# Kernel optimization log

Hardware: AMD Instinct MI355X
Metric: run time of the kernel (lower is better)

The kernel has to match this reference:

```python
import jax, jax.numpy as jnp
import numpy as np

N_NODES = 50000
N_EDGES = 1600000
IN_DIM = 128
HIDDEN = 256
N_CLASSES = 2
N_GRAPHS = 512
BN_EPS = 1e-5


def setup_inputs() -> dict:
    key = jax.random.key(0)
    ks = jax.random.split(key, 12)
    x = jax.random.normal(ks[0], (N_NODES, IN_DIM), dtype=jnp.float32)
    edge_index = jax.random.randint(ks[1], (2, N_EDGES), 0, N_NODES, dtype=jnp.int64)
    batch = jnp.sort(jax.random.randint(ks[2], (N_NODES,), 0, N_GRAPHS, dtype=jnp.int64))
    s1 = 1.0 / np.sqrt(IN_DIM)
    s2 = 1.0 / np.sqrt(HIDDEN)
    return {
        "x": x,
        "edge_index": edge_index,
        "batch": batch,
        # GIN MLP: Linear(in,hidden) -> BN -> ReLU -> Linear(hidden,hidden)
        "W1": jax.random.uniform(ks[3], (IN_DIM, HIDDEN), jnp.float32, -s1, s1),
        "b1": jnp.zeros((HIDDEN,), jnp.float32),
        "g1": jnp.ones((HIDDEN,), jnp.float32),
        "be1": jnp.zeros((HIDDEN,), jnp.float32),
        "W2": jax.random.uniform(ks[4], (HIDDEN, HIDDEN), jnp.float32, -s2, s2),
        "b2": jnp.zeros((HIDDEN,), jnp.float32),
        # attention gate: Linear(hidden, 1)
        "Wg": jax.random.uniform(ks[5], (HIDDEN, 1), jnp.float32, -s2, s2),
        "bg": jnp.zeros((1,), jnp.float32),
        # head: BN(hidden) -> Dropout(eval: identity) -> Linear(hidden, n_classes)
        "g2": jnp.ones((HIDDEN,), jnp.float32),
        "be2": jnp.zeros((HIDDEN,), jnp.float32),
        "Wh": jax.random.uniform(ks[6], (HIDDEN, N_CLASSES), jnp.float32, -s2, s2),
        "bh": jnp.zeros((N_CLASSES,), jnp.float32),
    }


def _batchnorm(h, gamma, beta):
    # training-mode BN: batch statistics over axis 0 (biased variance, as torch)
    mu = jnp.mean(h, axis=0)
    var = jnp.mean(jnp.square(h - mu), axis=0)
    return gamma * (h - mu) * jax.lax.rsqrt(var + BN_EPS) + beta


def reference(x, edge_index, batch, W1, b1, g1, be1, W2, b2, Wg, bg, g2, be2, Wh, bh):
    src, dst = edge_index[0], edge_index[1]
    # GINConv (eps=0): agg_i = sum_{j->i} x_j ; h = MLP(x + agg)
    agg = jax.ops.segment_sum(x[src], dst, num_segments=N_NODES)  # [N, in_dim]
    h = x + agg
    h = h @ W1 + b1                      # [N, hidden]
    h = jax.nn.relu(_batchnorm(h, g1, be1))
    h = h @ W2 + b2                      # [N, hidden]
    h = jax.nn.relu(h)                   # outer F.relu in forward
    # AttentionalAggregation: segment softmax of gate, weighted sum per graph
    gate = h @ Wg + bg                   # [N, 1]
    m = jax.ops.segment_max(gate, batch, num_segments=N_GRAPHS)  # [G, 1]
    e = jnp.exp(gate - m[batch])
    s = jax.ops.segment_sum(e, batch, num_segments=N_GRAPHS)     # [G, 1]
    alpha = e / s[batch]                 # [N, 1]
    pooled = jax.ops.segment_sum(alpha * h, batch, num_segments=N_GRAPHS)  # [G, hidden]
    # head: BN -> (Dropout eval = identity) -> Linear -> log_softmax
    z = _batchnorm(pooled, g2, be2) @ Wh + bh  # [G, n_classes]
    return jax.nn.log_softmax(z, axis=-1)
```

## Files before the change

### kernel.cpp

```cpp
#include <hip/hip_runtime.h>

typedef unsigned int u32;
typedef unsigned short ushort_t;
typedef __attribute__((ext_vector_type(8))) short bf16x8;
typedef __attribute__((ext_vector_type(4))) float f32x4;

#define PCAP 3072
#define OVFCAP 1600000

__device__ __forceinline__ float bf2f_lo(u32 u){
  union{u32 i; float f;} v; v.i = u<<16; return v.f;
}
__device__ __forceinline__ float bf2f_hi(u32 u){
  union{u32 i; float f;} v; v.i = u & 0xFFFF0000u; return v.f;
}
__device__ __forceinline__ float bf2f_s(ushort_t u){
  union{u32 i; float f;} v; v.i = ((u32)u)<<16; return v.f;
}
__device__ __forceinline__ u32 pack2bf(float a, float b){
  union{float f; u32 i;} va, vb; va.f=a; vb.f=b;
  u32 ra = (va.i + 0x7FFF + ((va.i>>16)&1)) >> 16;
  u32 rb = (vb.i + 0x7FFF + ((vb.i>>16)&1)) & 0xFFFF0000u;
  return ra | rb;
}
__device__ __forceinline__ ushort_t f2bf1(float f){
  union{float f; u32 i;} v; v.f=f;
  u32 r = v.i + 0x7FFF + ((v.i>>16)&1);
  return (ushort_t)(r>>16);
}

__global__ __launch_bounds__(256) void prep(const float* __restrict__ x, u32* __restrict__ xb, long nconv,
                                            const float* __restrict__ W1, ushort_t* __restrict__ W1t,
                                            const float* __restrict__ W2, ushort_t* __restrict__ W2t,
                                            int* __restrict__ bcursor, int* __restrict__ ovf_cnt, int NB){
  long blk = blockIdx.x;
  int tid = threadIdx.x;
  if(blk < nconv){
    long i = blk*256 + tid;
    float4 v = ((const float4*)x)[i];
    uint2 o; o.x = pack2bf(v.x, v.y); o.y = pack2bf(v.z, v.w);
    ((uint2*)xb)[i] = o;
  } else if(blk < nconv + 256){
    int n = (int)(blk - nconv);
    for(int k = tid; k < 128; k += 256) W1t[(size_t)n*128 + k] = f2bf1(W1[(size_t)k*256 + n]);
  } else if(blk < nconv + 512){
    int n = (int)(blk - nconv - 256);
    for(int k = tid; k < 256; k += 256) W2t[(size_t)n*256 + k] = f2bf1(W2[(size_t)k*256 + n]);
  } else {
    for(int i = tid; i < NB*16; i += 256) bcursor[i] = 0;
    if(tid == 0) *ovf_cnt = 0;
  }
}

__global__ __launch_bounds__(256) void binscatter_direct(const int* __restrict__ src, const int* __restrict__ dst,
                                                         int* __restrict__ bcursor, u32* __restrict__ pairs,
                                                         int* __restrict__ ovf, int* __restrict__ ovf_cnt,
                                                         int E, int N, int NB){
  __shared__ int hist[1024];
  __shared__ int base[1024];
  int e0 = blockIdx.x*8192;
  int e1 = min(e0+8192, E);
  for(int i=threadIdx.x; i<NB; i+=256) hist[i]=0;
  __syncthreads();
  for(int i=e0+threadIdx.x; i<e1; i+=256){
    int d = dst[i];
    if((u32)d >= (u32)N) d = 0;
    atomicAdd(&hist[d>>6], 1);
  }
  __syncthreads();
  for(int i=threadIdx.x; i<NB; i+=256){
    int c = hist[i];
    base[i] = c ? atomicAdd(&bcursor[i*16], c) : 0;
    hist[i] = 0;
  }
  __syncthreads();
  for(int i=e0+threadIdx.x; i<e1; i+=256){
    int d = dst[i]; if((u32)d >= (u32)N) d = 0;
    int s = src[i]; if((u32)s >= (u32)N) s = 0;
    int b = d>>6;
    int loc = atomicAdd(&hist[b], 1);
    int pos = base[b] + loc;
    if(pos < PCAP){
      pairs[(size_t)b*PCAP + pos] = (u32)s | (((u32)(d & 63))<<17);
    } else {
      int o = atomicAdd(ovf_cnt, 1);
      if(o < OVFCAP){ ovf[2*o] = s; ovf[2*o+1] = d; }
    }
  }
}

__global__ __launch_bounds__(512) void gather_bucket(const u32* __restrict__ xb,
                                                     const u32* __restrict__ pairs,
                                                     const int* __restrict__ bcursor,
                                                     const int* __restrict__ ovf, const int* __restrict__ ovf_cnt,
                                                     u32* __restrict__ h0b, int N){
  __shared__ int lsrc[PCAP];
  __shared__ int dcnt[64];
  __shared__ int dstart[65];
  __shared__ int dcur[64];
  __shared__ int s_ovfn;
  int b = blockIdx.x;
  int tid = threadIdx.x;
  int cnt = bcursor[b*16];
  if(cnt < 0) cnt = 0;
  int cl = min(cnt, PCAP);
  if(tid < 64) dcnt[tid] = 0;
  if(tid == 0){ int o = *ovf_cnt; s_ovfn = (o < 0) ? 0 : min(o, OVFCAP); }
  __syncthreads();
  const u32* mypairs = pairs + (size_t)b*PCAP;
  for(int i=tid; i<cl; i+=512){
    u32 u = mypairs[i];
    atomicAdd(&dcnt[(u>>17)&63], 1);
  }
  __syncthreads();
  if(tid==0){
    int run=0;
    #pragma unroll
    for(int j=0;j<64;j++){ dstart[j]=run; dcur[j]=run; run+=dcnt[j]; }
    dstart[64]=run;
  }
  __syncthreads();
  for(int i=tid; i<cl; i+=512){
    u32 u = mypairs[i];
    int pos = atomicAdd(&dcur[(u>>17)&63], 1);
    lsrc[pos] = (int)(u & 0x1FFFFu);
  }
  __syncthreads();
  int ovfn = s_ovfn;
  const uint4* xr = (const uint4*)xb;
  int slot = tid >> 4;
  int c = tid & 15;
  for(int pass=0; pass<2; pass++){
    int r = pass*32 + slot;
    int node = b*64 + r;
    if(node >= N) continue;
    uint4 xv = xr[(size_t)node*16 + c];
    float acc[8] = {
      bf2f_lo(xv.x), bf2f_hi(xv.x), bf2f_lo(xv.y), bf2f_hi(xv.y),
      bf2f_lo(xv.z), bf2f_hi(xv.z), bf2f_lo(xv.w), bf2f_hi(xv.w) };
    int ds = dstart[r], de = dstart[r+1];
    int j = ds;
    for(; j+8 <= de; j += 8){
      int s0=lsrc[j+0], s1=lsrc[j+1], s2=lsrc[j+2], s3=lsrc[j+3];
      int s4=lsrc[j+4], s5=lsrc[j+5], s6=lsrc[j+6], s7=lsrc[j+7];
      uint4 v0 = xr[(size_t)s0*16 + c];
      uint4 v1 = xr[(size_t)s1*16 + c];
      uint4 v2 = xr[(size_t)s2*16 + c];
      uint4 v3 = xr[(size_t)s3*16 + c];
      uint4 v4 = xr[(size_t)s4*16 + c];
      uint4 v5 = xr[(size_t)s5*16 + c];
      uint4 v6 = xr[(size_t)s6*16 + c];
      uint4 v7 = xr[(size_t)s7*16 + c];
      acc[0]+=bf2f_lo(v0.x)+bf2f_lo(v1.x)+bf2f_lo(v2.x)+bf2f_lo(v3.x)
             +bf2f_lo(v4.x)+bf2f_lo(v5.x)+bf2f_lo(v6.x)+bf2f_lo(v7.x);
      acc[1]+=bf2f_hi(v0.x)+bf2f_hi(v1.x)+bf2f_hi(v2.x)+bf2f_hi(v3.x)
             +bf2f_hi(v4.x)+bf2f_hi(v5.x)+bf2f_hi(v6.x)+bf2f_hi(v7.x);
      acc[2]+=bf2f_lo(v0.y)+bf2f_lo(v1.y)+bf2f_lo(v2.y)+bf2f_lo(v3.y)
             +bf2f_lo(v4.y)+bf2f_lo(v5.y)+bf2f_lo(v6.y)+bf2f_lo(v7.y);
      acc[3]+=bf2f_hi(v0.y)+bf2f_hi(v1.y)+bf2f_hi(v2.y)+bf2f_hi(v3.y)
             +bf2f_hi(v4.y)+bf2f_hi(v5.y)+bf2f_hi(v6.y)+bf2f_hi(v7.y);
      acc[4]+=bf2f_lo(v0.z)+bf2f_lo(v1.z)+bf2f_lo(v2.z)+bf2f_lo(v3.z)
             +bf2f_lo(v4.z)+bf2f_lo(v5.z)+bf2f_lo(v6.z)+bf2f_lo(v7.z);
      acc[5]+=bf2f_hi(v0.z)+bf2f_hi(v1.z)+bf2f_hi(v2.z)+bf2f_hi(v3.z)
             +bf2f_hi(v4.z)+bf2f_hi(v5.z)+bf2f_hi(v6.z)+bf2f_hi(v7.z);
      acc[6]+=bf2f_lo(v0.w)+bf2f_lo(v1.w)+bf2f_lo(v2.w)+bf2f_lo(v3.w)
             +bf2f_lo(v4.w)+bf2f_lo(v5.w)+bf2f_lo(v6.w)+bf2f_lo(v7.w);
      acc[7]+=bf2f_hi(v0.w)+bf2f_hi(v1.w)+bf2f_hi(v2.w)+bf2f_hi(v3.w)
             +bf2f_hi(v4.w)+bf2f_hi(v5.w)+bf2f_hi(v6.w)+bf2f_hi(v7.w);
    }
    for(; j < de; j++){
      int s = lsrc[j];
      uint4 v = xr[(size_t)s*16 + c];
      acc[0]+=bf2f_lo(v.x); acc[1]+=bf2f_hi(v.x);
      acc[2]+=bf2f_lo(v.y); acc[3]+=bf2f_hi(v.y);
      acc[4]+=bf2f_lo(v.z); acc[5]+=bf2f_hi(v.z);
      acc[6]+=bf2f_lo(v.w); acc[7]+=bf2f_hi(v.w);
    }
    if(ovfn > 0){
      for(int i=0;i<ovfn;i++){
        int s = ovf[2*i], d = ovf[2*i+1];
        if(d == node){
          if((u32)s >= (u32)N) s = 0;
          uint4 v = xr[(size_t)s*16 + c];
          acc[0]+=bf2f_lo(v.x); acc[1]+=bf2f_hi(v.x);
          acc[2]+=bf2f_lo(v.y); acc[3]+=bf2f_hi(v.y);
          acc[4]+=bf2f_lo(v.z); acc[5]+=bf2f_hi(v.z);
          acc[6]+=bf2f_lo(v.w); acc[7]+=bf2f_hi(v.w);
        }
      }
    }
    uint4 o;
    o.x = pack2bf(acc[0],acc[1]); o.y = pack2bf(acc[2],acc[3]);
    o.z = pack2bf(acc[4],acc[5]); o.w = pack2bf(acc[6],acc[7]);
    ((uint4*)h0b)[(size_t)node*16 + c] = o;
  }
}

template<int K, bool BNA, bool RELUOUT, bool GATE, bool ABF16, bool OUTBF16, bool STATS>
__global__ __launch_bounds__(512) void gemm_mfma(const void* __restrict__ Ap, const ushort_t* __restrict__ Wt,
                                                 const float* __restrict__ bias,
                                                 const float* __restrict__ scale, const float* __restrict__ shift,
                                                 void* __restrict__ Cp, int M,
                                                 const float* __restrict__ Wg, const float* __restrict__ bg,
                                                 float* __restrict__ gate,
                                                 float* __restrict__ psum, float* __restrict__ pq, int NS){
  __shared__ uint4 Al[8*129];
  __shared__ uint4 Bl[8*257];
  __shared__ float gacc[128];
  __shared__ float sstat[512];
  const int tid  = threadIdx.x;
  const int lane = tid & 63;
  const int wave = tid >> 6;
  const int lm   = lane & 15;
  const int q    = lane >> 4;
  const int mhalf= wave >> 2;
  const int nq   = wave & 3;
  const int m0   = blockIdx.x * 128;

  if(GATE && tid < 128) gacc[tid] = 0.f;
  if(STATS){ sstat[tid] = 0.f; }

  f32x4 acc[4][4];
  #pragma unroll
  for(int i=0;i<4;i++)
    #pragma unroll
    for(int j=0;j<4;j++) acc[i][j] = (f32x4){0.f,0.f,0.f,0.f};

  for(int k0=0; k0<K; k0+=64){
    #pragma unroll
    for(int i=0;i<2;i++){
      int idx = tid*2 + i;
      int m = idx >> 3, c = idx & 7;
      int grow = m0 + m;
      int kk = k0 + c*8;
      uint4 v = make_uint4(0,0,0,0);
      if(ABF16){
        if(grow < M) v = *(const uint4*)((const ushort_t*)Ap + (size_t)grow*K + kk);
        if(BNA){
          float f0=bf2f_lo(v.x), f1=bf2f_hi(v.x), f2=bf2f_lo(v.y), f3=bf2f_hi(v.y);
          float f4=bf2f_lo(v.z), f5=bf2f_hi(v.z), f6=bf2f_lo(v.w), f7=bf2f_hi(v.w);
          float4 s0 = *(const float4*)(scale+kk),  s1 = *(const float4*)(scale+kk+4);
          float4 t0 = *(const float4*)(shift+kk),  t1 = *(const float4*)(shift+kk+4);
          f0=fmaxf(fmaf(s0.x,f0,t0.x),0.f); f1=fmaxf(fmaf(s0.y,f1,t0.y),0.f);
          f2=fmaxf(fmaf(s0.z,f2,t0.z),0.f); f3=fmaxf(fmaf(s0.w,f3,t0.w),0.f);
          f4=fmaxf(fmaf(s1.x,f4,t1.x),0.f); f5=fmaxf(fmaf(s1.y,f5,t1.y),0.f);
          f6=fmaxf(fmaf(s1.z,f6,t1.z),0.f); f7=fmaxf(fmaf(s1.w,f7,t1.w),0.f);
          v.x = pack2bf(f0,f1); v.y = pack2bf(f2,f3);
          v.z = pack2bf(f4,f5); v.w = pack2bf(f6,f7);
        }
      } else {
        float4 u0 = make_float4(0,0,0,0), u1 = make_float4(0,0,0,0);
        if(grow < M){
          u0 = *(const float4*)((const float*)Ap + (size_t)grow*K + kk);
          u1 = *(const float4*)((const float*)Ap + (size_t)grow*K + kk + 4);
        }
        if(BNA){
          float4 s0 = *(const float4*)(scale+kk),  s1 = *(const float4*)(scale+kk+4);
          float4 t0 = *(const float4*)(shift+kk),  t1 = *(const float4*)(shift+kk+4);
          u0.x=fmaxf(fmaf(s0.x,u0.x,t0.x),0.f); u0.y=fmaxf(fmaf(s0.y,u0.y,t0.y),0.f);
          u0.z=fmaxf(fmaf(s0.z,u0.z,t0.z),0.f); u0.w=fmaxf(fmaf(s0.w,u0.w,t0.w),0.f);
          u1.x=fmaxf(fmaf(s1.x,u1.x,t1.x),0.f); u1.y=fmaxf(fmaf(s1.y,u1.y,t1.y),0.f);
          u1.z=fmaxf(fmaf(s1.z,u1.z,t1.z),0.f); u1.w=fmaxf(fmaf(s1.w,u1.w,t1.w),0.f);
        }
        v.x = pack2bf(u0.x,u0.y); v.y = pack2bf(u0.z,u0.w);
        v.z = pack2bf(u1.x,u1.y); v.w = pack2bf(u1.z,u1.w);
      }
      Al[c*129 + m] = v;
    }
    #pragma unroll
    for(int i=0;i<4;i++){
      int idx = tid*4 + i;
      int n = idx >> 3, c = idx & 7;
      Bl[c*257 + n] = *(const uint4*)(Wt + (size_t)n*K + k0 + c*8);
    }
    __syncthreads();
    #pragma unroll
    for(int ks=0; ks<2; ks++){
      int cc = ks*4 + q;
      bf16x8 af[4], bfr[4];
      #pragma unroll
      for(int mi=0; mi<4; mi++)
        af[mi] = *((const bf16x8*)&Al[cc*129 + mhalf*64 + mi*16 + lm]);
      #pragma unroll
      for(int ni=0; ni<4; ni++)
        bfr[ni] = *((const bf16x8*)&Bl[cc*257 + nq*64 + ni*16 + lm]);
      #pragma unroll
      for(int mi=0; mi<4; mi++)
        #pragma unroll
        for(int ni=0; ni<4; ni++)
          acc[mi][ni] = __builtin_amdgcn_mfma_f32_16x16x32_bf16(af[mi], bfr[ni], acc[mi][ni], 0, 0, 0);
    }
    __syncthreads();
  }

  float bb[4], wgv[4];
  float cs[4] = {0.f,0.f,0.f,0.f};
  float cq[4] = {0.f,0.f,0.f,0.f};
  #pragma unroll
  for(int ni=0; ni<4; ni++){
    int col = nq*64 + ni*16 + lm;
    bb[ni] = bias[col];
    if(GATE) wgv[ni] = Wg[col];
  }
  #pragma unroll
  for(int mi=0; mi<4; mi++){
    int rowloc0 = mhalf*64 + mi*16 + q*4;
    float gp[4] = {0.f,0.f,0.f,0.f};
    #pragma unroll
    for(int ni=0; ni<4; ni++){
      int col = nq*64 + ni*16 + lm;
      f32x4 o = acc[mi][ni];
      #pragma unroll
      for(int r=0; r<4; r++){
        float v = o[r] + bb[ni];
        if(RELUOUT) v = fmaxf(v, 0.f);
        int row = m0 + rowloc0 + r;
        if(row < M){
          if(OUTBF16) ((ushort_t*)Cp)[(size_t)row*256 + col] = f2bf1(v);
          else        ((float*)Cp)[(size_t)row*256 + col] = v;
          if(STATS){ cs[ni] += v; cq[ni] = fmaf(v, v, cq[ni]); }
        }
        if(GATE) gp[r] = fmaf(v, wgv[ni], gp[r]);
      }
    }
    if(GATE){
      #pragma unroll
      for(int r=0; r<4; r++){
        if(m0 + rowloc0 + r < M) atomicAdd(&gacc[rowloc0 + r], gp[r]);
      }
    }
  }
  if(STATS){
    __syncthreads();
    #pragma unroll
    for(int ni=0; ni<4; ni++){
      int col = nq*64 + ni*16 + lm;
      atomicAdd(&sstat[col], cs[ni]);
      atomicAdd(&sstat[256+col], cq[ni]);
    }
    __syncthreads();
    if(tid < 256){
      psum[(size_t)tid*NS + blockIdx.x] = sstat[tid];
      pq[(size_t)tid*NS + blockIdx.x]   = sstat[256+tid];
    }
  }
  if(GATE){
    __syncthreads();
    if(tid < 128){
      int row = m0 + tid;
      if(row < M) gate[row] = gacc[tid] + bg[0];
    }
  }
}

__global__ __launch_bounds__(256) void col_stats2(const float* __restrict__ h, float* __restrict__ psum,
                                                  float* __restrict__ pq, int M, int rpb, int nblk){
  int b = blockIdx.x;
  int g = threadIdx.x >> 6;
  int lane = threadIdx.x & 63;
  int c0 = lane*4;
  int r0 = b*rpb;
  int r1 = min(r0+rpb, M);
  float4 s4 = make_float4(0.f,0.f,0.f,0.f);
  float4 q4 = make_float4(0.f,0.f,0.f,0.f);
  for(int r=r0+g; r<r1; r+=4){
    float4 v = *(const float4*)(h + (size_t)r*256 + c0);
    s4.x+=v.x; s4.y+=v.y; s4.z+=v.z; s4.w+=v.w;
    q4.x=fmaf(v.x,v.x,q4.x); q4.y=fmaf(v.y,v.y,q4.y);
    q4.z=fmaf(v.z,v.z,q4.z); q4.w=fmaf(v.w,v.w,q4.w);
  }
  __shared__ float ls[1024];
  __shared__ float lq[1024];
  *(float4*)&ls[g*256+c0] = s4;
  *(float4*)&lq[g*256+c0] = q4;
  __syncthreads();
  if(threadIdx.x < 64){
    #pragma unroll
    for(int j=0;j<4;j++){
      int c = c0+j;
      float s = ls[c]+ls[256+c]+ls[512+c]+ls[768+c];
      float q = lq[c]+lq[256+c]+lq[512+c]+lq[768+c];
      psum[(size_t)c*nblk + b] = s;
      pq[(size_t)c*nblk + b]   = q;
    }
  }
}

__global__ __launch_bounds__(512) void stats_fin(const float* __restrict__ psum, const float* __restrict__ pq,
                                                 const float* __restrict__ gamma, const float* __restrict__ beta,
                                                 float* __restrict__ scale, float* __restrict__ shift,
                                                 int nblk, int NS, float invM){
  __shared__ float red[512];
  int t = threadIdx.x;
  const float* src = (t<256) ? (psum + (size_t)t*NS) : (pq + (size_t)(t-256)*NS);
  float s = 0.f;
  int i = 0;
  for(; i+4 <= nblk; i += 4){
    float4 v = *(const float4*)(src+i);
    s += v.x+v.y+v.z+v.w;
  }
  for(; i < nblk; i++) s += src[i];
  red[t]=s; __syncthreads();
  if(t<256){
    float mu  = red[t]*invM;
    float var = fmaxf(red[256+t]*invM - mu*mu, 0.f);
    float sc  = gamma[t] * rsqrtf(var + 1e-5f);
    scale[t]=sc; shift[t]=fmaf(-mu, sc, beta[t]);
  }
}

__global__ __launch_bounds__(512) void pool_k(const ushort_t* __restrict__ h2b, const float* __restrict__ gate,
                                              const int* __restrict__ batch, float* __restrict__ pooled, int N){
  int g = blockIdx.x;
  __shared__ int sb[2];
  __shared__ float red[8];
  __shared__ float s_m, s_inv;
  __shared__ float la[256];
  __shared__ float sa0[512];
  __shared__ float sa1[512];
  int t = threadIdx.x;
  if(t < 2){
    int target = g + t;
    int lo=0, hi=N;
    while(lo<hi){ int mid=(lo+hi)>>1; if(batch[mid] < target) lo=mid+1; else hi=mid; }
    sb[t] = lo;
  }
  __syncthreads();
  int beg = sb[0], end = sb[1];
  float mx = -1e30f;
  for(int i=beg+t; i<end; i+=512) mx = fmaxf(mx, gate[i]);
  #pragma unroll
  for(int d=32; d>0; d>>=1) mx = fmaxf(mx, __shfl_down(mx, d, 64));
  if((t&63)==0) red[t>>6] = mx;
  __syncthreads();
  if(t==0){
    float m = red[0];
    #pragma unroll
    for(int w=1; w<8; w++) m = fmaxf(m, red[w]);
    s_m = m;
  }
  __syncthreads();
  float m = s_m;
  float s = 0.f;
  for(int i=beg+t; i<end; i+=512) s += expf(gate[i]-m);
  #pragma unroll
  for(int d=32; d>0; d>>=1) s += __shfl_down(s, d, 64);
  if((t&63)==0) red[t>>6] = s;
  __syncthreads();
  if(t==0){
    float tot = 0.f;
    #pragma unroll
    for(int w=0; w<8; w++) tot += red[w];
    s_inv = (tot > 0.f) ? 1.f/tot : 0.f;
  }
  __syncthreads();
  float inv = s_inv;
  const u32* h2w = (const u32*)h2b;
  int colpair = t & 127;
  int rowgrp  = t >> 7;
  float a0 = 0.f, a1 = 0.f;
  for(int ci=beg; ci<end; ci+=256){
    int chunk = min(256, end-ci);
    if(t < 256) la[t] = (t < chunk) ? expf(gate[ci+t]-m)*inv : 0.f;
    __syncthreads();
    for(int j=rowgrp; j<chunk; j+=4){
      u32 h = h2w[(size_t)(ci+j)*128 + colpair];
      float w = la[j];
      a0 = fmaf(w, bf2f_lo(h), a0);
      a1 = fmaf(w, bf2f_hi(h), a1);
    }
    __syncthreads();
  }
  sa0[t] = a0; sa1[t] = a1;
  __syncthreads();
  if(t < 128){
    float r0 = sa0[t] + sa0[128+t] + sa0[256+t] + sa0[384+t];
    float r1 = sa1[t] + sa1[128+t] + sa1[256+t] + sa1[384+t];
    pooled[g*256 + t*2]   = r0;
    pooled[g*256 + t*2+1] = r1;
  }
}

__global__ __launch_bounds__(256) void head_k(const float* __restrict__ pooled,
                                              const float* __restrict__ sc2, const float* __restrict__ sh2,
                                              const float* __restrict__ Wh, const float* __restrict__ bh,
                                              float* __restrict__ out, int G){
  int w = (blockIdx.x*256 + threadIdx.x) >> 6;
  int l = threadIdx.x & 63;
  if(w >= G) return;
  float4 v  = *(const float4*)(pooled + (size_t)w*256 + l*4);
  float4 sc = *(const float4*)(sc2 + l*4);
  float4 sh = *(const float4*)(sh2 + l*4);
  float vv[4] = { fmaf(sc.x,v.x,sh.x), fmaf(sc.y,v.y,sh.y), fmaf(sc.z,v.z,sh.z), fmaf(sc.w,v.w,sh.w) };
  float4 w0 = *(const float4*)(Wh + (size_t)l*8);
  float4 w1 = *(const float4*)(Wh + (size_t)l*8 + 4);
  float a0 = vv[0]*w0.x + vv[1]*w0.z + vv[2]*w1.x + vv[3]*w1.z;
  float a1 = vv[0]*w0.y + vv[1]*w0.w + vv[2]*w1.y + vv[3]*w1.w;
  #pragma unroll
  for(int d=32; d>0; d>>=1){ a0 += __shfl_down(a0,d,64); a1 += __shfl_down(a1,d,64); }
  if(l==0){
    float z0 = a0 + bh[0];
    float z1 = a1 + bh[1];
    float mz = fmaxf(z0,z1);
    float lse = mz + logf(expf(z0-mz) + expf(z1-mz));
    out[w*2]   = z0 - lse;
    out[w*2+1] = z1 - lse;
  }
}

extern "C" void kernel_launch(void* const* d_in, const int* in_sizes, int n_in,
                              void* d_out, int out_size, void* d_ws, size_t ws_size,
                              hipStream_t stream){
  const float* x   = (const float*)d_in[0];
  const int*   ei  = (const int*)d_in[1];
  const int*   bat = (const int*)d_in[2];
  const float* W1  = (const float*)d_in[3];
  const float* b1  = (const float*)d_in[4];
  const float* g1  = (const float*)d_in[5];
  const float* be1 = (const float*)d_in[6];
  const float* W2  = (const float*)d_in[7];
  const float* b2  = (const float*)d_in[8];
  const float* Wg  = (const float*)d_in[9];
  const float* bg  = (const float*)d_in[10];
  const float* g2  = (const float*)d_in[11];
  const float* be2 = (const float*)d_in[12];
  const float* Wh  = (const float*)d_in[13];
  const float* bh  = (const float*)d_in[14];

  const int N = in_sizes[0] / 128;
  const int E = in_sizes[1] / 2;
  const int G = out_size / 2;
  const int NB = (N + 63) >> 6;
  const int gblocks = (N + 127)/128;
  const int NS1 = (gblocks + 7) & ~7;
  const int NBLK2 = 64;

  char* ws = (char*)d_ws;
  u32*   h0b    = (u32*)ws;
  u32*   xb     = (u32*)(ws + 12800000);
  u32*   pairs  = (u32*)(ws + 25600000);
  int*   bcursor= (int*)(ws + 35210240);
  int*   ovf_cnt= (int*)(ws + 35275776);
  int*   ovf    = (int*)(ws + 35276032);
  ushort_t* h2b = (ushort_t*)ws;
  u32*   h1b    = (u32*)(ws + 51200000);
  char*  p2 = ws + 102400000;
  float* psum1 = (float*)p2;          p2 += 256*NS1*4;
  float* pq1   = (float*)p2;          p2 += 256*NS1*4;
  float* psum2 = (float*)p2;          p2 += 256*NBLK2*4;
  float* pq2   = (float*)p2;          p2 += 256*NBLK2*4;
  float* sc1   = (float*)p2;          p2 += 1024;
  float* sh1   = (float*)p2;          p2 += 1024;
  float* sc2   = (float*)p2;          p2 += 1024;
  float* sh2   = (float*)p2;          p2 += 1024;
  float* gate  = (float*)p2;          p2 += (size_t)N*4 + 4096;
  float* pooled= (float*)p2;          p2 += (size_t)G*256*4;
  ushort_t* W1t = (ushort_t*)p2;      p2 += 256*128*2;
  ushort_t* W2t = (ushort_t*)p2;      p2 += 256*256*2;

  const int* src = ei;
  const int* dst = ei + E;

  long nconv = (long)N*128/4/256;
  prep<<<(int)(nconv + 512 + 1), 256, 0, stream>>>(x, xb, nconv, W1, W1t, W2, W2t, bcursor, ovf_cnt, NB);

  int nchunk = (E + 8191)/8192;
  binscatter_direct<<<nchunk, 256, 0, stream>>>(src, dst, bcursor, pairs, ovf, ovf_cnt, E, N, NB);
  gather_bucket<<<NB, 512, 0, stream>>>(xb, pairs, bcursor, ovf, ovf_cnt, h0b, N);

  gemm_mfma<128,false,false,false,true,true,true><<<gblocks, 512, 0, stream>>>(
      h0b, W1t, b1, nullptr, nullptr, h1b, N, nullptr, nullptr, nullptr, psum1, pq1, NS1);
  stats_fin<<<1, 512, 0, stream>>>(psum1, pq1, g1, be1, sc1, sh1, gblocks, NS1, 1.0f/(float)N);
  gemm_mfma<256,true,true,true,true,true,false><<<gblocks, 512, 0, stream>>>(
      h1b, W2t, b2, sc1, sh1, h2b, N, Wg, bg, gate, nullptr, nullptr, 0);

  pool_k<<<G, 512, 0, stream>>>(h2b, gate, bat, pooled, N);
  int rpb2 = (G + NBLK2 - 1)/NBLK2;
  col_stats2<<<NBLK2, 256, 0, stream>>>(pooled, psum2, pq2, G, rpb2, NBLK2);
  stats_fin<<<1, 512, 0, stream>>>(psum2, pq2, g2, be2, sc2, sh2, NBLK2, NBLK2, 1.0f/(float)G);
  head_k<<<(G+3)/4, 256, 0, stream>>>(pooled, sc2, sh2, Wh, bh, (float*)d_out, G);
}
```

Measured before the change: 343.8 us.

## Fuse pipeline into one cooperative persistent megakernel with grid syncs

```diff
diff --git a/kernel.cpp b/kernel.cpp
--- a/kernel.cpp
+++ b/kernel.cpp
@@ -1,4 +1,7 @@
 #include <hip/hip_runtime.h>
+#include <hip/hip_cooperative_groups.h>
+
+namespace cg = cooperative_groups;
 
 typedef unsigned int u32;
 typedef unsigned short ushort_t;
@@ -13,9 +16,6 @@
 }
 __device__ __forceinline__ float bf2f_hi(u32 u){
   union{u32 i; float f;} v; v.i = u & 0xFFFF0000u; return v.f;
-}
-__device__ __forceinline__ float bf2f_s(ushort_t u){
-  union{u32 i; float f;} v; v.i = ((u32)u)<<16; return v.f;
 }
 __device__ __forceinline__ u32 pack2bf(float a, float b){
   union{float f; u32 i;} va, vb; va.f=a; vb.f=b;
@@ -29,57 +29,41 @@
   return (ushort_t)(r>>16);
 }
 
-__global__ __launch_bounds__(256) void prep(const float* __restrict__ x, u32* __restrict__ xb, long nconv,
-                                            const float* __restrict__ W1, ushort_t* __restrict__ W1t,
-                                            const float* __restrict__ W2, ushort_t* __restrict__ W2t,
-                                            int* __restrict__ bcursor, int* __restrict__ ovf_cnt, int NB){
-  long blk = blockIdx.x;
+struct GemmSM { uint4 Al[8*129]; uint4 Bl[8*257]; float gacc[128]; float sstat[512]; };
+struct GatherSM { int lsrc[PCAP]; int dcnt[64]; int dstart[65]; int dcur[64]; int ovfn; };
+struct ScatSM { int hist[1024]; int base[1024]; };
+struct PoolSM { int sb[2]; float red[8]; float m, inv; float la[256]; float sa0[512]; float sa1[512]; };
+struct PStatSM { float ls[2048]; float lq[2048]; };
+union SM {
+  GemmSM g; GatherSM ga; ScatSM s; PoolSM p; PStatSM ps; float red512[512];
+};
+
+
+__device__ void binscatter_chunk(SM& sm, int ch, const int* src, const int* dst,
+                                 int* bcursor, u32* pairs, int* ovf, int* ovf_cnt,
+                                 int E, int N, int NB){
   int tid = threadIdx.x;
-  if(blk < nconv){
-    long i = blk*256 + tid;
-    float4 v = ((const float4*)x)[i];
-    uint2 o; o.x = pack2bf(v.x, v.y); o.y = pack2bf(v.z, v.w);
-    ((uint2*)xb)[i] = o;
-  } else if(blk < nconv + 256){
-    int n = (int)(blk - nconv);
-    for(int k = tid; k < 128; k += 256) W1t[(size_t)n*128 + k] = f2bf1(W1[(size_t)k*256 + n]);
-  } else if(blk < nconv + 512){
-    int n = (int)(blk - nconv - 256);
-    for(int k = tid; k < 256; k += 256) W2t[(size_t)n*256 + k] = f2bf1(W2[(size_t)k*256 + n]);
-  } else {
-    for(int i = tid; i < NB*16; i += 256) bcursor[i] = 0;
-    if(tid == 0) *ovf_cnt = 0;
-  }
-}
-
-__global__ __launch_bounds__(256) void binscatter_direct(const int* __restrict__ src, const int* __restrict__ dst,
-                                                         int* __restrict__ bcursor, u32* __restrict__ pairs,
-                                                         int* __restrict__ ovf, int* __restrict__ ovf_cnt,
-                                                         int E, int N, int NB){
-  __shared__ int hist[1024];
-  __shared__ int base[1024];
-  int e0 = blockIdx.x*8192;
-  int e1 = min(e0+8192, E);
-  for(int i=threadIdx.x; i<NB; i+=256) hist[i]=0;
-  __syncthreads();
-  for(int i=e0+threadIdx.x; i<e1; i+=256){
+  int e0 = ch*8192, e1 = min(e0+8192, E);
+  for(int i=tid;i<NB;i+=512) sm.s.hist[i]=0;
+  __syncthreads();
+  for(int i=e0+tid;i<e1;i+=512){
     int d = dst[i];
     if((u32)d >= (u32)N) d = 0;
-    atomicAdd(&hist[d>>6], 1);
-  }
-  __syncthreads();
-  for(int i=threadIdx.x; i<NB; i+=256){
-    int c = hist[i];
-    base[i] = c ? atomicAdd(&bcursor[i*16], c) : 0;
-    hist[i] = 0;
-  }
-  __syncthreads();
-  for(int i=e0+threadIdx.x; i<e1; i+=256){
+    atomicAdd(&sm.s.hist[d>>6], 1);
+  }
+  __syncthreads();
+  for(int i=tid;i<NB;i+=512){
+    int c = sm.s.hist[i];
+    sm.s.base[i] = c ? atomicAdd(&bcursor[i*16], c) : 0;
+    sm.s.hist[i] = 0;
+  }
+  __syncthreads();
+  for(int i=e0+tid;i<e1;i+=512){
     int d = dst[i]; if((u32)d >= (u32)N) d = 0;
     int s = src[i]; if((u32)s >= (u32)N) s = 0;
     int b = d>>6;
-    int loc = atomicAdd(&hist[b], 1);
-    int pos = base[b] + loc;
+    int loc = atomicAdd(&sm.s.hist[b], 1);
+    int pos = sm.s.base[b] + loc;
     if(pos < PCAP){
       pairs[(size_t)b*PCAP + pos] = (u32)s | (((u32)(d & 63))<<17);
     } else {
@@ -87,46 +71,39 @@
       if(o < OVFCAP){ ovf[2*o] = s; ovf[2*o+1] = d; }
     }
   }
-}
-
-__global__ __launch_bounds__(512) void gather_bucket(const u32* __restrict__ xb,
-                                                     const u32* __restrict__ pairs,
-                                                     const int* __restrict__ bcursor,
-                                                     const int* __restrict__ ovf, const int* __restrict__ ovf_cnt,
-                                                     u32* __restrict__ h0b, int N){
-  __shared__ int lsrc[PCAP];
-  __shared__ int dcnt[64];
-  __shared__ int dstart[65];
-  __shared__ int dcur[64];
-  __shared__ int s_ovfn;
-  int b = blockIdx.x;
+  __syncthreads();
+}
+
+__device__ void gather_one(SM& sm, int b, const u32* xb, const u32* pairs,
+                           const int* bcursor, const int* ovf, const int* ovf_cnt,
+                           u32* h0b, int N){
   int tid = threadIdx.x;
   int cnt = bcursor[b*16];
   if(cnt < 0) cnt = 0;
   int cl = min(cnt, PCAP);
-  if(tid < 64) dcnt[tid] = 0;
-  if(tid == 0){ int o = *ovf_cnt; s_ovfn = (o < 0) ? 0 : min(o, OVFCAP); }
+  if(tid < 64) sm.ga.dcnt[tid] = 0;
+  if(tid == 0){ int o = *ovf_cnt; sm.ga.ovfn = (o < 0) ? 0 : min(o, OVFCAP); }
   __syncthreads();
   const u32* mypairs = pairs + (size_t)b*PCAP;
   for(int i=tid; i<cl; i+=512){
     u32 u = mypairs[i];
-    atomicAdd(&dcnt[(u>>17)&63], 1);
+    atomicAdd(&sm.ga.dcnt[(u>>17)&63], 1);
   }
   __syncthreads();
   if(tid==0){
     int run=0;
     #pragma unroll
-    for(int j=0;j<64;j++){ dstart[j]=run; dcur[j]=run; run+=dcnt[j]; }
-    dstart[64]=run;
+    for(int j=0;j<64;j++){ sm.ga.dstart[j]=run; sm.ga.dcur[j]=run; run+=sm.ga.dcnt[j]; }
+    sm.ga.dstart[64]=run;
   }
   __syncthreads();
   for(int i=tid; i<cl; i+=512){
     u32 u = mypairs[i];
-    int pos = atomicAdd(&dcur[(u>>17)&63], 1);
-    lsrc[pos] = (int)(u & 0x1FFFFu);
-  }
-  __syncthreads();
-  int ovfn = s_ovfn;
+    int pos = atomicAdd(&sm.ga.dcur[(u>>17)&63], 1);
+    sm.ga.lsrc[pos] = (int)(u & 0x1FFFFu);
+  }
+  __syncthreads();
+  int ovfn = sm.ga.ovfn;
   const uint4* xr = (const uint4*)xb;
   int slot = tid >> 4;
   int c = tid & 15;
@@ -138,11 +115,11 @@
     float acc[8] = {
       bf2f_lo(xv.x), bf2f_hi(xv.x), bf2f_lo(xv.y), bf2f_hi(xv.y),
       bf2f_lo(xv.z), bf2f_hi(xv.z), bf2f_lo(xv.w), bf2f_hi(xv.w) };
-    int ds = dstart[r], de = dstart[r+1];
+    int ds = sm.ga.dstart[r], de = sm.ga.dstart[r+1];
     int j = ds;
     for(; j+8 <= de; j += 8){
-      int s0=lsrc[j+0], s1=lsrc[j+1], s2=lsrc[j+2], s3=lsrc[j+3];
-      int s4=lsrc[j+4], s5=lsrc[j+5], s6=lsrc[j+6], s7=lsrc[j+7];
+      int s0=sm.ga.lsrc[j+0], s1=sm.ga.lsrc[j+1], s2=sm.ga.lsrc[j+2], s3=sm.ga.lsrc[j+3];
+      int s4=sm.ga.lsrc[j+4], s5=sm.ga.lsrc[j+5], s6=sm.ga.lsrc[j+6], s7=sm.ga.lsrc[j+7];
       uint4 v0 = xr[(size_t)s0*16 + c];
       uint4 v1 = xr[(size_t)s1*16 + c];
       uint4 v2 = xr[(size_t)s2*16 + c];
@@ -169,7 +146,7 @@
              +bf2f_hi(v4.w)+bf2f_hi(v5.w)+bf2f_hi(v6.w)+bf2f_hi(v7.w);
     }
     for(; j < de; j++){
-      int s = lsrc[j];
+      int s = sm.ga.lsrc[j];
       uint4 v = xr[(size_t)s*16 + c];
       acc[0]+=bf2f_lo(v.x); acc[1]+=bf2f_hi(v.x);
       acc[2]+=bf2f_lo(v.y); acc[3]+=bf2f_hi(v.y);
@@ -194,20 +171,14 @@
     o.z = pack2bf(acc[4],acc[5]); o.w = pack2bf(acc[6],acc[7]);
     ((uint4*)h0b)[(size_t)node*16 + c] = o;
   }
-}
-
-template<int K, bool BNA, bool RELUOUT, bool GATE, bool ABF16, bool OUTBF16, bool STATS>
-__global__ __launch_bounds__(512) void gemm_mfma(const void* __restrict__ Ap, const ushort_t* __restrict__ Wt,
-                                                 const float* __restrict__ bias,
-                                                 const float* __restrict__ scale, const float* __restrict__ shift,
-                                                 void* __restrict__ Cp, int M,
-                                                 const float* __restrict__ Wg, const float* __restrict__ bg,
-                                                 float* __restrict__ gate,
-                                                 float* __restrict__ psum, float* __restrict__ pq, int NS){
-  __shared__ uint4 Al[8*129];
-  __shared__ uint4 Bl[8*257];
-  __shared__ float gacc[128];
-  __shared__ float sstat[512];
+  __syncthreads();
+}
+
+template<int K, bool BNA, bool RELUOUT, bool GATE, bool STATS>
+__device__ void gemm_tile(SM& sm, int tile, const ushort_t* Ap, const ushort_t* Wt,
+                          const float* bias, const float* scale, const float* shift,
+                          ushort_t* Cp, int M, const float* Wg, const float* bg,
+                          float* gate, float* psum, float* pq, int NS){
   const int tid  = threadIdx.x;
   const int lane = tid & 63;
   const int wave = tid >> 6;
@@ -215,10 +186,10 @@
   const int q    = lane >> 4;
   const int mhalf= wave >> 2;
   const int nq   = wave & 3;
-  const int m0   = blockIdx.x * 128;
-
-  if(GATE && tid < 128) gacc[tid] = 0.f;
-  if(STATS){ sstat[tid] = 0.f; }
+  const int m0   = tile * 128;
+
+  if(GATE && tid < 128) sm.g.gacc[tid] = 0.f;
+  if(STATS) sm.g.sstat[tid] = 0.f;
 
   f32x4 acc[4][4];
   #pragma unroll
@@ -234,44 +205,26 @@
       int grow = m0 + m;
       int kk = k0 + c*8;
       uint4 v = make_uint4(0,0,0,0);
-      if(ABF16){
-        if(grow < M) v = *(const uint4*)((const ushort_t*)Ap + (size_t)grow*K + kk);
-        if(BNA){
-          float f0=bf2f_lo(v.x), f1=bf2f_hi(v.x), f2=bf2f_lo(v.y), f3=bf2f_hi(v.y);
-          float f4=bf2f_lo(v.z), f5=bf2f_hi(v.z), f6=bf2f_lo(v.w), f7=bf2f_hi(v.w);
-          float4 s0 = *(const float4*)(scale+kk),  s1 = *(const float4*)(scale+kk+4);
-          float4 t0 = *(const float4*)(shift+kk),  t1 = *(const float4*)(shift+kk+4);
-          f0=fmaxf(fmaf(s0.x,f0,t0.x),0.f); f1=fmaxf(fmaf(s0.y,f1,t0.y),0.f);
-          f2=fmaxf(fmaf(s0.z,f2,t0.z),0.f); f3=fmaxf(fmaf(s0.w,f3,t0.w),0.f);
-          f4=fmaxf(fmaf(s1.x,f4,t1.x),0.f); f5=fmaxf(fmaf(s1.y,f5,t1.y),0.f);
-          f6=fmaxf(fmaf(s1.z,f6,t1.z),0.f); f7=fmaxf(fmaf(s1.w,f7,t1.w),0.f);
-          v.x = pack2bf(f0,f1); v.y = pack2bf(f2,f3);
-          v.z = pack2bf(f4,f5); v.w = pack2bf(f6,f7);
-        }
-      } else {
-        float4 u0 = make_float4(0,0,0,0), u1 = make_float4(0,0,0,0);
-        if(grow < M){
-          u0 = *(const float4*)((const float*)Ap + (size_t)grow*K + kk);
-          u1 = *(const float4*)((const float*)Ap + (size_t)grow*K + kk + 4);
-        }
-        if(BNA){
-          float4 s0 = *(const float4*)(scale+kk),  s1 = *(const float4*)(scale+kk+4);
-          float4 t0 = *(const float4*)(shift+kk),  t1 = *(const float4*)(shift+kk+4);
-          u0.x=fmaxf(fmaf(s0.x,u0.x,t0.x),0.f); u0.y=fmaxf(fmaf(s0.y,u0.y,t0.y),0.f);
-          u0.z=fmaxf(fmaf(s0.z,u0.z,t0.z),0.f); u0.w=fmaxf(fmaf(s0.w,u0.w,t0.w),0.f);
-          u1.x=fmaxf(fmaf(s1.x,u1.x,t1.x),0.f); u1.y=fmaxf(fmaf(s1.y,u1.y,t1.y),0.f);
-          u1.z=fmaxf(fmaf(s1.z,u1.z,t1.z),0.f); u1.w=fmaxf(fmaf(s1.w,u1.w,t1.w),0.f);
-        }
-        v.x = pack2bf(u0.x,u0.y); v.y = pack2bf(u0.z,u0.w);
-        v.z = pack2bf(u1.x,u1.y); v.w = pack2bf(u1.z,u1.w);
+      if(grow < M) v = *(const uint4*)(Ap + (size_t)grow*K + kk);
+      if(BNA){
+        float f0=bf2f_lo(v.x), f1=bf2f_hi(v.x), f2=bf2f_lo(v.y), f3=bf2f_hi(v.y);
+        float f4=bf2f_lo(v.z), f5=bf2f_hi(v.z), f6=bf2f_lo(v.w), f7=bf2f_hi(v.w);
+        float4 s0 = *(const float4*)(scale+kk),  s1 = *(const float4*)(scale+kk+4);
+        float4 t0 = *(const float4*)(shift+kk),  t1 = *(const float4*)(shift+kk+4);
+        f0=fmaxf(fmaf(s0.x,f0,t0.x),0.f); f1=fmaxf(fmaf(s0.y,f1,t0.y),0.f);
+        f2=fmaxf(fmaf(s0.z,f2,t0.z),0.f); f3=fmaxf(fmaf(s0.w,f3,t0.w),0.f);
+        f4=fmaxf(fmaf(s1.x,f4,t1.x),0.f); f5=fmaxf(fmaf(s1.y,f5,t1.y),0.f);
+        f6=fmaxf(fmaf(s1.z,f6,t1.z),0.f); f7=fmaxf(fmaf(s1.w,f7,t1.w),0.f);
+        v.x = pack2bf(f0,f1); v.y = pack2bf(f2,f3);
+        v.z = pack2bf(f4,f5); v.w = pack2bf(f6,f7);
       }
-      Al[c*129 + m] = v;
+      sm.g.Al[c*129 + m] = v;
     }
     #pragma unroll
     for(int i=0;i<4;i++){
       int idx = tid*4 + i;
       int n = idx >> 3, c = idx & 7;
-      Bl[c*257 + n] = *(const uint4*)(Wt + (size_t)n*K + k0 + c*8);
+      sm.g.Bl[c*257 + n] = *(const uint4*)(Wt + (size_t)n*K + k0 + c*8);
     }
     __syncthreads();
     #pragma unroll
@@ -280,10 +233,10 @@
       bf16x8 af[4], bfr[4];
       #pragma unroll
       for(int mi=0; mi<4; mi++)
-        af[mi] = *((const bf16x8*)&Al[cc*129 + mhalf*64 + mi*16 + lm]);
+        af[mi] = *((const bf16x8*)&sm.g.Al[cc*129 + mhalf*64 + mi*16 + lm]);
       #pragma unroll
       for(int ni=0; ni<4; ni++)
-        bfr[ni] = *((const bf16x8*)&Bl[cc*257 + nq*64 + ni*16 + lm]);
+        bfr[ni] = *((const bf16x8*)&sm.g.Bl[cc*257 + nq*64 + ni*16 + lm]);
       #pragma unroll
       for(int mi=0; mi<4; mi++)
         #pragma unroll
@@ -316,8 +269,7 @@
         if(RELUOUT) v = fmaxf(v, 0.f);
         int row = m0 + rowloc0 + r;
         if(row < M){
-          if(OUTBF16) ((ushort_t*)Cp)[(size_t)row*256 + col] = f2bf1(v);
-          else        ((float*)Cp)[(size_t)row*256 + col] = v;
+          Cp[(size_t)row*256 + col] = f2bf1(v);
           if(STATS){ cs[ni] += v; cq[ni] = fmaf(v, v, cq[ni]); }
         }
         if(GATE) gp[r] = fmaf(v, wgv[ni], gp[r]);
@@ -326,7 +278,7 @@
     if(GATE){
       #pragma unroll
       for(int r=0; r<4; r++){
-        if(m0 + rowloc0 + r < M) atomicAdd(&gacc[rowloc0 + r], gp[r]);
+        if(m0 + rowloc0 + r < M) atomicAdd(&sm.g.gacc[rowloc0 + r], gp[r]);
       }
     }
   }
@@ -335,62 +287,28 @@
     #pragma unroll
     for(int ni=0; ni<4; ni++){
       int col = nq*64 + ni*16 + lm;
-      atomicAdd(&sstat[col], cs[ni]);
-      atomicAdd(&sstat[256+col], cq[ni]);
+      atomicAdd(&sm.g.sstat[col], cs[ni]);
+      atomicAdd(&sm.g.sstat[256+col], cq[ni]);
     }
     __syncthreads();
     if(tid < 256){
-      psum[(size_t)tid*NS + blockIdx.x] = sstat[tid];
-      pq[(size_t)tid*NS + blockIdx.x]   = sstat[256+tid];
+      psum[(size_t)tid*NS + tile] = sm.g.sstat[tid];
+      pq[(size_t)tid*NS + tile]   = sm.g.sstat[256+tid];
     }
   }
   if(GATE){
     __syncthreads();
     if(tid < 128){
       int row = m0 + tid;
-      if(row < M) gate[row] = gacc[tid] + bg[0];
-    }
-  }
-}
-
-__global__ __launch_bounds__(256) void col_stats2(const float* __restrict__ h, float* __restrict__ psum,
-                                                  float* __restrict__ pq, int M, int rpb, int nblk){
-  int b = blockIdx.x;
-  int g = threadIdx.x >> 6;
-  int lane = threadIdx.x & 63;
-  int c0 = lane*4;
-  int r0 = b*rpb;
-  int r1 = min(r0+rpb, M);
-  float4 s4 = make_float4(0.f,0.f,0.f,0.f);
-  float4 q4 = make_float4(0.f,0.f,0.f,0.f);
-  for(int r=r0+g; r<r1; r+=4){
-    float4 v = *(const float4*)(h + (size_t)r*256 + c0);
-    s4.x+=v.x; s4.y+=v.y; s4.z+=v.z; s4.w+=v.w;
-    q4.x=fmaf(v.x,v.x,q4.x); q4.y=fmaf(v.y,v.y,q4.y);
-    q4.z=fmaf(v.z,v.z,q4.z); q4.w=fmaf(v.w,v.w,q4.w);
-  }
-  __shared__ float ls[1024];
-  __shared__ float lq[1024];
-  *(float4*)&ls[g*256+c0] = s4;
-  *(float4*)&lq[g*256+c0] = q4;
-  __syncthreads();
-  if(threadIdx.x < 64){
-    #pragma unroll
-    for(int j=0;j<4;j++){
-      int c = c0+j;
-      float s = ls[c]+ls[256+c]+ls[512+c]+ls[768+c];
-      float q = lq[c]+lq[256+c]+lq[512+c]+lq[768+c];
-      psum[(size_t)c*nblk + b] = s;
-      pq[(size_t)c*nblk + b]   = q;
-    }
-  }
-}
-
-__global__ __launch_bounds__(512) void stats_fin(const float* __restrict__ psum, const float* __restrict__ pq,
-                                                 const float* __restrict__ gamma, const float* __restrict__ beta,
-                                                 float* __restrict__ scale, float* __restrict__ shift,
-                                                 int nblk, int NS, float invM){
-  __shared__ float red[512];
+      if(row < M) gate[row] = sm.g.gacc[tid] + bg[0];
+    }
+  }
+  __syncthreads();
+}
+
+__device__ void stats_fin_dev(float* red, const float* psum, const float* pq,
+                              const float* gamma, const float* beta,
+                              float* scale, float* shift, int nblk, int NS, float invM){
   int t = threadIdx.x;
   const float* src = (t<256) ? (psum + (size_t)t*NS) : (pq + (size_t)(t-256)*NS);
   float s = 0.f;
@@ -407,87 +325,102 @@
     float sc  = gamma[t] * rsqrtf(var + 1e-5f);
     scale[t]=sc; shift[t]=fmaf(-mu, sc, beta[t]);
   }
-}
-
-__global__ __launch_bounds__(512) void pool_k(const ushort_t* __restrict__ h2b, const float* __restrict__ gate,
-                                              const int* __restrict__ batch, float* __restrict__ pooled, int N){
-  int g = blockIdx.x;
-  __shared__ int sb[2];
-  __shared__ float red[8];
-  __shared__ float s_m, s_inv;
-  __shared__ float la[256];
-  __shared__ float sa0[512];
-  __shared__ float sa1[512];
+  __syncthreads();
+}
+
+__device__ void pool_one(SM& sm, int g, const ushort_t* h2b, const float* gate,
+                         const int* batch, float* pooled, int N){
   int t = threadIdx.x;
   if(t < 2){
     int target = g + t;
     int lo=0, hi=N;
     while(lo<hi){ int mid=(lo+hi)>>1; if(batch[mid] < target) lo=mid+1; else hi=mid; }
-    sb[t] = lo;
-  }
-  __syncthreads();
-  int beg = sb[0], end = sb[1];
+    sm.p.sb[t] = lo;
+  }
+  __syncthreads();
+  int beg = sm.p.sb[0], end = sm.p.sb[1];
   float mx = -1e30f;
   for(int i=beg+t; i<end; i+=512) mx = fmaxf(mx, gate[i]);
   #pragma unroll
   for(int d=32; d>0; d>>=1) mx = fmaxf(mx, __shfl_down(mx, d, 64));
-  if((t&63)==0) red[t>>6] = mx;
+  if((t&63)==0) sm.p.red[t>>6] = mx;
   __syncthreads();
   if(t==0){
-    float m = red[0];
-    #pragma unroll
-    for(int w=1; w<8; w++) m = fmaxf(m, red[w]);
-    s_m = m;
-  }
-  __syncthreads();
-  float m = s_m;
+    float m = sm.p.red[0];
+    #pragma unroll
+    for(int w=1; w<8; w++) m = fmaxf(m, sm.p.red[w]);
+    sm.p.m = m;
+  }
+  __syncthreads();
+  float m = sm.p.m;
   float s = 0.f;
   for(int i=beg+t; i<end; i+=512) s += expf(gate[i]-m);
   #pragma unroll
   for(int d=32; d>0; d>>=1) s += __shfl_down(s, d, 64);
-  if((t&63)==0) red[t>>6] = s;
+  if((t&63)==0) sm.p.red[t>>6] = s;
   __syncthreads();
   if(t==0){
     float tot = 0.f;
     #pragma unroll
-    for(int w=0; w<8; w++) tot += red[w];
-    s_inv = (tot > 0.f) ? 1.f/tot : 0.f;
-  }
-  __syncthreads();
-  float inv = s_inv;
+    for(int w=0; w<8; w++) tot += sm.p.red[w];
+    sm.p.inv = (tot > 0.f) ? 1.f/tot : 0.f;
+  }
+  __syncthreads();
+  float inv = sm.p.inv;
   const u32* h2w = (const u32*)h2b;
   int colpair = t & 127;
   int rowgrp  = t >> 7;
   float a0 = 0.f, a1 = 0.f;
   for(int ci=beg; ci<end; ci+=256){
     int chunk = min(256, end-ci);
-    if(t < 256) la[t] = (t < chunk) ? expf(gate[ci+t]-m)*inv : 0.f;
+    if(t < 256) sm.p.la[t] = (t < chunk) ? expf(gate[ci+t]-m)*inv : 0.f;
     __syncthreads();
     for(int j=rowgrp; j<chunk; j+=4){
       u32 h = h2w[(size_t)(ci+j)*128 + colpair];
-      float w = la[j];
+      float w = sm.p.la[j];
       a0 = fmaf(w, bf2f_lo(h), a0);
       a1 = fmaf(w, bf2f_hi(h), a1);
     }
     __syncthreads();
   }
-  sa0[t] = a0; sa1[t] = a1;
+  sm.p.sa0[t] = a0; sm.p.sa1[t] = a1;
   __syncthreads();
   if(t < 128){
-    float r0 = sa0[t] + sa0[128+t] + sa0[256+t] + sa0[384+t];
-    float r1 = sa1[t] + sa1[128+t] + sa1[256+t] + sa1[384+t];
+    float r0 = sm.p.sa0[t] + sm.p.sa0[128+t] + sm.p.sa0[256+t] + sm.p.sa0[384+t];
+    float r1 = sm.p.sa1[t] + sm.p.sa1[128+t] + sm.p.sa1[256+t] + sm.p.sa1[384+t];
     pooled[g*256 + t*2]   = r0;
     pooled[g*256 + t*2+1] = r1;
   }
-}
-
-__global__ __launch_bounds__(256) void head_k(const float* __restrict__ pooled,
-                                              const float* __restrict__ sc2, const float* __restrict__ sh2,
-                                              const float* __restrict__ Wh, const float* __restrict__ bh,
-                                              float* __restrict__ out, int G){
-  int w = (blockIdx.x*256 + threadIdx.x) >> 6;
+  __syncthreads();
+}
+
+__device__ void pstat_one(SM& sm, int b, const float* pooled, float* psum2, float* pq2, int G){
+  int t = threadIdx.x;
+  int grp = t >> 6, lane = t & 63, c0 = lane*4;
+  int r = b*8 + grp;
+  float4 v = make_float4(0,0,0,0);
+  if(r < G) v = *(const float4*)(pooled + (size_t)r*256 + c0);
+  *(float4*)&sm.ps.ls[grp*256+c0] = v;
+  float4 q = make_float4(v.x*v.x, v.y*v.y, v.z*v.z, v.w*v.w);
+  *(float4*)&sm.ps.lq[grp*256+c0] = q;
+  __syncthreads();
+  if(t < 64){
+    #pragma unroll
+    for(int j=0;j<4;j++){
+      int c = c0+j;
+      float s=0.f, qq=0.f;
+      #pragma unroll
+      for(int gi=0; gi<8; gi++){ s += sm.ps.ls[gi*256+c]; qq += sm.ps.lq[gi*256+c]; }
+      psum2[(size_t)c*64 + b] = s;
+      pq2[(size_t)c*64 + b]   = qq;
+    }
+  }
+  __syncthreads();
+}
+
+__device__ void head_one(int w, const float* pooled, const float* sc2, const float* sh2,
+                         const float* Wh, const float* bh, float* out){
   int l = threadIdx.x & 63;
-  if(w >= G) return;
   float4 v  = *(const float4*)(pooled + (size_t)w*256 + l*4);
   float4 sc = *(const float4*)(sc2 + l*4);
   float4 sh = *(const float4*)(sh2 + l*4);
@@ -508,24 +441,138 @@
   }
 }
 
+struct MP {
+  const float *x, *W1, *b1, *g1, *be1, *W2, *b2, *Wg, *bg, *g2, *be2, *Wh, *bh;
+  const int *src, *dst, *bat;
+  u32 *xb, *h0b, *pairs, *h1b;
+  ushort_t *h2b, *W1t, *W2t;
+  int *bcursor, *ovf, *ovf_cnt;
+  float *psum1,*pq1,*psum2,*pq2,*sc1,*sh1,*sc2,*sh2,*gate,*pooled,*out;
+  int N,E,G,NB,gblocks,NS1,nchunk;
+};
+
+__global__ __launch_bounds__(512, 4) void mega(MP p){
+  cg::grid_group grid = cg::this_grid();
+  __shared__ SM sm;
+  int bid = blockIdx.x, nb = gridDim.x, tid = threadIdx.x;
+
+  {
+    long total = (long)p.N*32;
+    for(long i=(long)bid*512+tid; i<total; i+=(long)nb*512){
+      float4 v = ((const float4*)p.x)[i];
+      uint2 o; o.x = pack2bf(v.x, v.y); o.y = pack2bf(v.z, v.w);
+      ((uint2*)p.xb)[i] = o;
+    }
+    for(int i=bid*512+tid; i<256*128; i+=nb*512){
+      int n=i>>7, k=i&127;
+      p.W1t[(size_t)n*128+k] = f2bf1(p.W1[(size_t)k*256+n]);
+    }
+    for(int i=bid*512+tid; i<256*256; i+=nb*512){
+      int n=i>>8, k=i&255;
+      p.W2t[(size_t)n*256+k] = f2bf1(p.W2[(size_t)k*256+n]);
+    }
+    for(int i=bid*512+tid; i<p.NB*16; i+=nb*512) p.bcursor[i]=0;
+    if(bid==0 && tid==0) *p.ovf_cnt = 0;
+  }
+  grid.sync();
+  for(int ch=bid; ch<p.nchunk; ch+=nb)
+    binscatter_chunk(sm, ch, p.src, p.dst, p.bcursor, p.pairs, p.ovf, p.ovf_cnt, p.E, p.N, p.NB);
+  grid.sync();
+  for(int b=bid; b<p.NB; b+=nb)
+    gather_one(sm, b, p.xb, p.pairs, p.bcursor, p.ovf, p.ovf_cnt, p.h0b, p.N);
+  grid.sync();
+  for(int t=bid; t<p.gblocks; t+=nb)
+    gemm_tile<128,false,false,false,true>(sm, t, (const ushort_t*)p.h0b, p.W1t, p.b1,
+        nullptr, nullptr, (ushort_t*)p.h1b, p.N, nullptr, nullptr, nullptr, p.psum1, p.pq1, p.NS1);
+  grid.sync();
+  if(bid==0) stats_fin_dev(sm.red512, p.psum1, p.pq1, p.g1, p.be1, p.sc1, p.sh1, p.gblocks, p.NS1, 1.0f/(float)p.N);
+  grid.sync();
+  for(int t=bid; t<p.gblocks; t+=nb)
+    gemm_tile<256,true,true,true,false>(sm, t, (const ushort_t*)p.h1b, p.W2t, p.b2,
+        p.sc1, p.sh1, p.h2b, p.N, p.Wg, p.bg, p.gate, nullptr, nullptr, 0);
+  grid.sync();
+  for(int g=bid; g<p.G; g+=nb)
+    pool_one(sm, g, p.h2b, p.gate, p.bat, p.pooled, p.N);
+  grid.sync();
+  if(bid < 64) pstat_one(sm, bid, p.pooled, p.psum2, p.pq2, p.G);
+  grid.sync();
+  if(bid==0) stats_fin_dev(sm.red512, p.psum2, p.pq2, p.g2, p.be2, p.sc2, p.sh2, 64, 64, 1.0f/(float)p.G);
+  grid.sync();
+  {
+    int w = bid*8 + (tid>>6);
+    if(w < p.G) head_one(w, p.pooled, p.sc2, p.sh2, p.Wh, p.bh, p.out);
+  }
+}
+
+__global__ __launch_bounds__(512) void k_prep(MP p){
+  int bid = blockIdx.x, nb = gridDim.x, tid = threadIdx.x;
+  long total = (long)p.N*32;
+  for(long i=(long)bid*512+tid; i<total; i+=(long)nb*512){
+    float4 v = ((const float4*)p.x)[i];
+    uint2 o; o.x = pack2bf(v.x, v.y); o.y = pack2bf(v.z, v.w);
+    ((uint2*)p.xb)[i] = o;
+  }
+  for(int i=bid*512+tid; i<256*128; i+=nb*512){
+    int n=i>>7, k=i&127;
+    p.W1t[(size_t)n*128+k] = f2bf1(p.W1[(size_t)k*256+n]);
+  }
+  for(int i=bid*512+tid; i<256*256; i+=nb*512){
+    int n=i>>8, k=i&255;
+    p.W2t[(size_t)n*256+k] = f2bf1(p.W2[(size_t)k*256+n]);
+  }
+  for(int i=bid*512+tid; i<p.NB*16; i+=nb*512) p.bcursor[i]=0;
+  if(bid==0 && tid==0) *p.ovf_cnt = 0;
+}
+__global__ __launch_bounds__(512) void k_binscatter(MP p){
+  __shared__ SM sm;
+  for(int ch=blockIdx.x; ch<p.nchunk; ch+=gridDim.x)
+    binscatter_chunk(sm, ch, p.src, p.dst, p.bcursor, p.pairs, p.ovf, p.ovf_cnt, p.E, p.N, p.NB);
+}
+__global__ __launch_bounds__(512) void k_gather(MP p){
+  __shared__ SM sm;
+  for(int b=blockIdx.x; b<p.NB; b+=gridDim.x)
+    gather_one(sm, b, p.xb, p.pairs, p.bcursor, p.ovf, p.ovf_cnt, p.h0b, p.N);
+}
+__global__ __launch_bounds__(512) void k_gemm1(MP p){
+  __shared__ SM sm;
+  for(int t=blockIdx.x; t<p.gblocks; t+=gridDim.x)
+    gemm_tile<128,false,false,false,true>(sm, t, (const ushort_t*)p.h0b, p.W1t, p.b1,
+        nullptr, nullptr, (ushort_t*)p.h1b, p.N, nullptr, nullptr, nullptr, p.psum1, p.pq1, p.NS1);
+}
+__global__ __launch_bounds__(512) void k_fin1(MP p){
+  __shared__ float red[512];
+  stats_fin_dev(red, p.psum1, p.pq1, p.g1, p.be1, p.sc1, p.sh1, p.gblocks, p.NS1, 1.0f/(float)p.N);
+}
+__global__ __launch_bounds__(512) void k_gemm2(MP p){
+  __shared__ SM sm;
+  for(int t=blockIdx.x; t<p.gblocks; t+=gridDim.x)
+    gemm_tile<256,true,true,true,false>(sm, t, (const ushort_t*)p.h1b, p.W2t, p.b2,
+        p.sc1, p.sh1, p.h2b, p.N, p.Wg, p.bg, p.gate, nullptr, nullptr, 0);
+}
+__global__ __launch_bounds__(512) void k_pool(MP p){
+  __shared__ SM sm;
+  for(int g=blockIdx.x; g<p.G; g+=gridDim.x)
+    pool_one(sm, g, p.h2b, p.gate, p.bat, p.pooled, p.N);
+}
+__global__ __launch_bounds__(512) void k_pstat(MP p){
+  __shared__ SM sm;
+  if(blockIdx.x < 64) pstat_one(sm, blockIdx.x, p.pooled, p.psum2, p.pq2, p.G);
+}
+__global__ __launch_bounds__(512) void k_fin2(MP p){
+  __shared__ float red[512];
+  stats_fin_dev(red, p.psum2, p.pq2, p.g2, p.be2, p.sc2, p.sh2, 64, 64, 1.0f/(float)p.G);
+}
+__global__ __launch_bounds__(512) void k_head(MP p){
+  int w = blockIdx.x*8 + (threadIdx.x>>6);
+  if(w < p.G) head_one(w, p.pooled, p.sc2, p.sh2, p.Wh, p.bh, p.out);
+}
+
 extern "C" void kernel_launch(void* const* d_in, const int* in_sizes, int n_in,
                               void* d_out, int out_size, void* d_ws, size_t ws_size,
                               hipStream_t stream){
   const float* x   = (const float*)d_in[0];
   const int*   ei  = (const int*)d_in[1];
   const int*   bat = (const int*)d_in[2];
-  const float* W1  = (const float*)d_in[3];
-  const float* b1  = (const float*)d_in[4];
-  const float* g1  = (const float*)d_in[5];
-  const float* be1 = (const float*)d_in[6];
-  const float* W2  = (const float*)d_in[7];
-  const float* b2  = (const float*)d_in[8];
-  const float* Wg  = (const float*)d_in[9];
-  const float* bg  = (const float*)d_in[10];
-  const float* g2  = (const float*)d_in[11];
-  const float* be2 = (const float*)d_in[12];
-  const float* Wh  = (const float*)d_in[13];
-  const float* bh  = (const float*)d_in[14];
 
   const int N = in_sizes[0] / 128;
   const int E = in_sizes[1] / 2;
@@ -533,50 +580,66 @@
   const int NB = (N + 63) >> 6;
   const int gblocks = (N + 127)/128;
   const int NS1 = (gblocks + 7) & ~7;
-  const int NBLK2 = 64;
 
   char* ws = (char*)d_ws;
-  u32*   h0b    = (u32*)ws;
-  u32*   xb     = (u32*)(ws + 12800000);
-  u32*   pairs  = (u32*)(ws + 25600000);
-  int*   bcursor= (int*)(ws + 35210240);
-  int*   ovf_cnt= (int*)(ws + 35275776);
-  int*   ovf    = (int*)(ws + 35276032);
-  ushort_t* h2b = (ushort_t*)ws;
-  u32*   h1b    = (u32*)(ws + 51200000);
-  char*  p2 = ws + 102400000;
-  float* psum1 = (float*)p2;          p2 += 256*NS1*4;
-  float* pq1   = (float*)p2;          p2 += 256*NS1*4;
-  float* psum2 = (float*)p2;          p2 += 256*NBLK2*4;
-  float* pq2   = (float*)p2;          p2 += 256*NBLK2*4;
-  float* sc1   = (float*)p2;          p2 += 1024;
-  float* sh1   = (float*)p2;          p2 += 1024;
-  float* sc2   = (float*)p2;          p2 += 1024;
-  float* sh2   = (float*)p2;          p2 += 1024;
-  float* gate  = (float*)p2;          p2 += (size_t)N*4 + 4096;
-  float* pooled= (float*)p2;          p2 += (size_t)G*256*4;
-  ushort_t* W1t = (ushort_t*)p2;      p2 += 256*128*2;
-  ushort_t* W2t = (ushort_t*)p2;      p2 += 256*256*2;
-
-  const int* src = ei;
-  const int* dst = ei + E;
-
-  long nconv = (long)N*128/4/256;
-  prep<<<(int)(nconv + 512 + 1), 256, 0, stream>>>(x, xb, nconv, W1, W1t, W2, W2t, bcursor, ovf_cnt, NB);
-
-  int nchunk = (E + 8191)/8192;
-  binscatter_direct<<<nchunk, 256, 0, stream>>>(src, dst, bcursor, pairs, ovf, ovf_cnt, E, N, NB);
-  gather_bucket<<<NB, 512, 0, stream>>>(xb, pairs, bcursor, ovf, ovf_cnt, h0b, N);
-
-  gemm_mfma<128,false,false,false,true,true,true><<<gblocks, 512, 0, stream>>>(
-      h0b, W1t, b1, nullptr, nullptr, h1b, N, nullptr, nullptr, nullptr, psum1, pq1, NS1);
-  stats_fin<<<1, 512, 0, stream>>>(psum1, pq1, g1, be1, sc1, sh1, gblocks, NS1, 1.0f/(float)N);
-  gemm_mfma<256,true,true,true,true,true,false><<<gblocks, 512, 0, stream>>>(
-      h1b, W2t, b2, sc1, sh1, h2b, N, Wg, bg, gate, nullptr, nullptr, 0);
-
-  pool_k<<<G, 512, 0, stream>>>(h2b, gate, bat, pooled, N);
-  int rpb2 = (G + NBLK2 - 1)/NBLK2;
-  col_stats2<<<NBLK2, 256, 0, stream>>>(pooled, psum2, pq2, G, rpb2, NBLK2);
-  stats_fin<<<1, 512, 0, stream>>>(psum2, pq2, g2, be2, sc2, sh2, NBLK2, NBLK2, 1.0f/(float)G);
-  head_k<<<(G+3)/4, 256, 0, stream>>>(pooled, sc2, sh2, Wh, bh, (float*)d_out, G);
-}
+  MP p;
+  p.x = x; p.src = ei; p.dst = ei + E; p.bat = bat;
+  p.W1 = (const float*)d_in[3]; p.b1 = (const float*)d_in[4];
+  p.g1 = (const float*)d_in[5]; p.be1 = (const float*)d_in[6];
+  p.W2 = (const float*)d_in[7]; p.b2 = (const float*)d_in[8];
+  p.Wg = (const float*)d_in[9]; p.bg = (const float*)d_in[10];
+  p.g2 = (const float*)d_in[11]; p.be2 = (const float*)d_in[12];
+  p.Wh = (const float*)d_in[13]; p.bh = (const float*)d_in[14];
+
+  p.h0b    = (u32*)ws;
+  p.xb     = (u32*)(ws + 12800000);
+  p.pairs  = (u32*)(ws + 25600000);
+  p.bcursor= (int*)(ws + 35210240);
+  p.ovf_cnt= (int*)(ws + 35275776);
+  p.ovf    = (int*)(ws + 35276032);
+  p.h2b    = (ushort_t*)ws;
+  p.h1b    = (u32*)(ws + 51200000);
+  char* p2 = ws + 102400000;
+  p.psum1 = (float*)p2;          p2 += 256*NS1*4;
+  p.pq1   = (float*)p2;          p2 += 256*NS1*4;
+  p.psum2 = (float*)p2;          p2 += 256*64*4;
+  p.pq2   = (float*)p2;          p2 += 256*64*4;
+  p.sc1   = (float*)p2;          p2 += 1024;
+  p.sh1   = (float*)p2;          p2 += 1024;
+  p.sc2   = (float*)p2;          p2 += 1024;
+  p.sh2   = (float*)p2;          p2 += 1024;
+  p.gate  = (float*)p2;          p2 += (size_t)N*4 + 4096;
+  p.pooled= (float*)p2;          p2 += (size_t)G*256*4;
+  p.W1t   = (ushort_t*)p2;       p2 += 256*128*2;
+  p.W2t   = (ushort_t*)p2;       p2 += 256*256*2;
+  p.out   = (float*)d_out;
+  p.N = N; p.E = E; p.G = G; p.NB = NB;
+  p.gblocks = gblocks; p.NS1 = NS1;
+  p.nchunk = (E + 8191)/8192;
+
+  int blocksPerCU = 0;
+  hipError_t qerr = hipOccupancyMaxActiveBlocksPerMultiprocessor(&blocksPerCU, (const void*)mega, 512, 0);
+  int grid = 0;
+  if(qerr == hipSuccess && blocksPerCU > 0){
+    grid = blocksPerCU * 256;
+    if(grid > 512) grid = 512;
+  }
+
+  hipError_t lerr = hipErrorUnknown;
+  if(grid >= 64){
+    void* kargs[] = { (void*)&p };
+    lerr = hipLaunchCooperativeKernel((const void*)mega, dim3(grid), dim3(512), kargs, 0, stream);
+  }
+  if(lerr != hipSuccess){
+    k_prep      <<<1024, 512, 0, stream>>>(p);
+    k_binscatter<<<p.nchunk, 512, 0, stream>>>(p);
+    k_gather    <<<NB, 512, 0, stream>>>(p);
+    k_gemm1     <<<gblocks, 512, 0, stream>>>(p);
+    k_fin1      <<<1, 512, 0, stream>>>(p);
+    k_gemm2     <<<gblocks, 512, 0, stream>>>(p);
+    k_pool      <<<G, 512, 0, stream>>>(p);
+    k_pstat     <<<64, 512, 0, stream>>>(p);
+    k_fin2      <<<1, 512, 0, stream>>>(p);
+    k_head      <<<(G+7)/8, 512, 0, stream>>>(p);
+  }
+}
```

New measurement: 375.4 us. 1.09x slower.
